# Optimization experiments

Measured on AMD Instinct MI355X. Metric: run time of the kernel, lower is better.

## Reference

```python
import jax, jax.numpy as jnp
import numpy as np

B, N, D_IN, D_OUT, H = 2, 2048, 1024, 1024, 16
HD = D_OUT // H


def setup_inputs() -> dict:
    key = jax.random.key(0)
    ks = jax.random.split(key, 6)
    s_in = 1.0 / np.sqrt(D_IN)
    s_out = 1.0 / np.sqrt(D_OUT)
    return {
        "x": jax.random.normal(ks[0], (B, N, D_IN), dtype=jnp.float32),
        "Wq": jax.random.uniform(ks[1], (D_IN, D_OUT), jnp.float32, -s_in, s_in),
        "Wk": jax.random.uniform(ks[2], (D_IN, D_OUT), jnp.float32, -s_in, s_in),
        "Wv": jax.random.uniform(ks[3], (D_IN, D_OUT), jnp.float32, -s_in, s_in),
        "Wo": jax.random.uniform(ks[4], (D_OUT, D_OUT), jnp.float32, -s_out, s_out),
        "bo": jax.random.uniform(ks[5], (D_OUT,), jnp.float32, -s_out, s_out),
    }


def reference(x, Wq, Wk, Wv, Wo, bo):
    b, n, _ = x.shape
    # project and split heads: [b, n, d_out] -> [b, h, n, hd]
    def heads(w):
        return w.reshape(b, n, H, HD).transpose(0, 2, 1, 3)
    q = heads(x @ Wq)
    k = heads(x @ Wk)
    v = heads(x @ Wv)
    # materialized causal attention (dropout rate 0.0 -> identity)
    scores = jnp.einsum("bhqd,bhkd->bhqk", q, k)
    causal = jnp.tril(jnp.ones((n, n), dtype=bool))  # keep lower triangle
    scores = jnp.where(causal, scores, -jnp.inf)
    attn = jax.nn.softmax(scores / np.sqrt(HD), axis=-1)
    ctx = jnp.einsum("bhqk,bhkd->bhqd", attn, v)
    ctx = ctx.transpose(0, 2, 1, 3).reshape(b, n, D_OUT)
    return ctx @ Wo + bo
```

## Files before the change

kernel.cpp:

```cpp
#include <hip/hip_runtime.h>
#include <math.h>
#include <stdint.h>

#define B_ 2
#define N_ 2048
#define D_ 1024
#define H_ 16
#define HD_ 64
#define M_ (B_ * N_)

typedef __bf16 bf16x8 __attribute__((ext_vector_type(8)));
typedef float f32x4 __attribute__((ext_vector_type(4)));

__device__ __forceinline__ ushort bfbits(float f) {
    __bf16 h = (__bf16)f;
    return __builtin_bit_cast(ushort, h);
}

__device__ __forceinline__ void glds16(const ushort* g, ushort* l) {
    __builtin_amdgcn_global_load_lds(
        (const __attribute__((address_space(1))) uint32_t*)g,
        (__attribute__((address_space(3))) uint32_t*)l, 16, 0, 0);
}

__global__ __launch_bounds__(256) void cvt_x(const float* __restrict__ x,
                                             ushort* __restrict__ xb) {
    int i = blockIdx.x * 256 + threadIdx.x;
    float4 v = ((const float4*)x)[i];
    ushort4 o;
    o.x = bfbits(v.x); o.y = bfbits(v.y); o.z = bfbits(v.z); o.w = bfbits(v.w);
    ((ushort4*)xb)[i] = o;
}

__global__ __launch_bounds__(256) void cvt_w(const float* __restrict__ W0,
                                             const float* __restrict__ W1,
                                             const float* __restrict__ W2,
                                             const float* __restrict__ W3,
                                             ushort* __restrict__ Wt) {
    __shared__ float T[32][33];
    const float* W = (blockIdx.z == 0) ? W0 : (blockIdx.z == 1) ? W1
                   : (blockIdx.z == 2) ? W2 : W3;
    ushort* out = Wt + (size_t)blockIdx.z * D_ * D_;
    const int t = threadIdx.x;
    const int k0 = blockIdx.x * 32, n0 = blockIdx.y * 32;
    {
        int kl = t >> 3, nl = (t & 7) * 4;
        float4 v = *(const float4*)&W[(size_t)(k0 + kl) * D_ + n0 + nl];
        T[kl][nl] = v.x; T[kl][nl + 1] = v.y; T[kl][nl + 2] = v.z; T[kl][nl + 3] = v.w;
    }
    __syncthreads();
    {
        int nl = t >> 3, k4 = (t & 7) * 4;
        ushort4 o;
        o.x = bfbits(T[k4 + 0][nl]); o.y = bfbits(T[k4 + 1][nl]);
        o.z = bfbits(T[k4 + 2][nl]); o.w = bfbits(T[k4 + 3][nl]);
        *(ushort4*)&out[(size_t)(n0 + nl) * D_ + k0 + k4] = o;
    }
}

#define BK 32

__device__ __forceinline__ void gemm_tile(const ushort* __restrict__ A,
                                          const ushort* __restrict__ Bt,
                                          int K, int tileM, int tileN,
                                          ushort* As, ushort* Bs,
                                          f32x4 acc[4][4]) {
    const int t = threadIdx.x;
    const int l = t & 63;
    const int w = __builtin_amdgcn_readfirstlane(t >> 6);
    const int wr = w >> 1, wc = w & 1;
    const int li = l & 15, lg = l >> 4;
    const int lr = l >> 2;
    const int colu = (((l & 3) ^ (lr & 3)) << 3);
    const int swz = (li & 3) << 3;

    for (int k0 = 0; k0 < K; k0 += BK) {
        __syncthreads();
        #pragma unroll
        for (int it = 0; it < 2; ++it) {
            const int c2 = it * 4 + w;
            const int row = c2 * 16 + lr;
            glds16(&A[(size_t)(tileM + row) * K + k0 + colu], &As[c2 * 512]);
            glds16(&Bt[(size_t)(tileN + row) * K + k0 + colu], &Bs[c2 * 512]);
        }
        __syncthreads();
        bf16x8 a[4], b[4];
        #pragma unroll
        for (int m = 0; m < 4; ++m)
            a[m] = *(const bf16x8*)&As[(wr * 64 + m * 16 + li) * 32 + ((lg << 3) ^ swz)];
        #pragma unroll
        for (int n = 0; n < 4; ++n)
            b[n] = *(const bf16x8*)&Bs[(wc * 64 + n * 16 + li) * 32 + ((lg << 3) ^ swz)];
        #pragma unroll
        for (int m = 0; m < 4; ++m)
            #pragma unroll
            for (int n = 0; n < 4; ++n)
                acc[m][n] = __builtin_amdgcn_mfma_f32_16x16x32_bf16(a[m], b[n], acc[m][n], 0, 0, 0);
    }
}

#define QSCALE 0.180336880f

__global__ __launch_bounds__(256) void qkv_gemm(const ushort* __restrict__ xb,
                                                const ushort* __restrict__ Wt,
                                                ushort* __restrict__ q,
                                                ushort* __restrict__ k,
                                                ushort* __restrict__ vt) {
    __shared__ ushort As[128 * 32];
    __shared__ ushort Bs[128 * 32];
    __shared__ ushort Eps[128][130];
    f32x4 acc[4][4];
    #pragma unroll
    for (int m = 0; m < 4; ++m)
        #pragma unroll
        for (int n = 0; n < 4; ++n)
            acc[m][n] = (f32x4){0.f, 0.f, 0.f, 0.f};

    const int tileM = blockIdx.x * 128;
    const int wsel = blockIdx.y >> 3;
    const int tileN = (blockIdx.y & 7) * 128;
    const ushort* Bmat = Wt + (size_t)wsel * D_ * D_;

    gemm_tile(xb, Bmat, D_, tileM, tileN, As, Bs, acc);

    const int t = threadIdx.x;
    const int l = t & 63, w = t >> 6;
    const int wr = w >> 1, wc = w & 1;
    const int li = l & 15, lg = l >> 4;
    const float scale = (wsel == 0) ? QSCALE : 1.0f;

    if (wsel < 2) {
        #pragma unroll
        for (int m = 0; m < 4; ++m)
            #pragma unroll
            for (int n = 0; n < 4; ++n)
                #pragma unroll
                for (int r = 0; r < 4; ++r)
                    Eps[wr * 64 + m * 16 + lg * 4 + r][wc * 64 + n * 16 + li] =
                        bfbits(acc[m][n][r] * scale);
    } else {
        #pragma unroll
        for (int m = 0; m < 4; ++m)
            #pragma unroll
            for (int n = 0; n < 4; ++n)
                #pragma unroll
                for (int r = 0; r < 4; ++r)
                    Eps[wc * 64 + n * 16 + li][wr * 64 + m * 16 + lg * 4 + r] =
                        bfbits(acc[m][n][r]);
    }
    __syncthreads();

    const int rr = t >> 3;
    const int cb = (t & 7) * 16;
    if (wsel < 2) {
        ushort* out = (wsel == 0) ? q : k;
        #pragma unroll
        for (int it = 0; it < 4; ++it) {
            const int row = it * 32 + rr;
            uint4 v0 = *(const uint4*)&Eps[row][cb];
            uint4 v1 = *(const uint4*)&Eps[row][cb + 8];
            size_t base = (size_t)(tileM + row) * D_ + tileN + cb;
            *(uint4*)&out[base] = v0;
            *(uint4*)&out[base + 8] = v1;
        }
    } else {
        const int b = tileM >> 11;
        const int n0 = (tileM & (N_ - 1)) + cb;
        #pragma unroll
        for (int it = 0; it < 4; ++it) {
            const int row = it * 32 + rr;
            const int gcol = tileN + row;
            const int h = gcol >> 6, hd = gcol & 63;
            uint4 v0 = *(const uint4*)&Eps[row][cb];
            uint4 v1 = *(const uint4*)&Eps[row][cb + 8];
            size_t base = ((size_t)(b * H_ + h) * HD_ + hd) * N_ + n0;
            *(uint4*)&vt[base] = v0;
            *(uint4*)&vt[base + 8] = v1;
        }
    }
}

__global__ __launch_bounds__(256) void out_gemm(const ushort* __restrict__ ctx,
                                                const ushort* __restrict__ Wt,
                                                const float* __restrict__ bo,
                                                float* __restrict__ outp) {
    __shared__ ushort As[128 * 32];
    __shared__ ushort Bs[128 * 32];
    __shared__ float Epf[32][132];
    f32x4 acc[4][4];
    #pragma unroll
    for (int m = 0; m < 4; ++m)
        #pragma unroll
        for (int n = 0; n < 4; ++n)
            acc[m][n] = (f32x4){0.f, 0.f, 0.f, 0.f};

    const int tileM = blockIdx.x * 128;
    const int tileN = blockIdx.y * 128;
    const ushort* Bmat = Wt + (size_t)3 * D_ * D_;

    gemm_tile(ctx, Bmat, D_, tileM, tileN, As, Bs, acc);

    const int t = threadIdx.x;
    const int l = t & 63, w = t >> 6;
    const int wr = w >> 1, wc = w & 1;
    const int li = l & 15, lg = l >> 4;
    const int lrow = t & 31;
    const int coff = (t >> 5) * 16;

    float bias[4];
    #pragma unroll
    for (int n = 0; n < 4; ++n) bias[n] = bo[tileN + wc * 64 + n * 16 + li];

    #pragma unroll
    for (int m = 0; m < 4; ++m) {
        __syncthreads();
        #pragma unroll
        for (int n = 0; n < 4; ++n)
            #pragma unroll
            for (int r = 0; r < 4; ++r)
                Epf[wr * 16 + lg * 4 + r][wc * 64 + n * 16 + li] = acc[m][n][r] + bias[n];
        __syncthreads();
        const int grow = tileM + (lrow >> 4) * 64 + m * 16 + (lrow & 15);
        #pragma unroll
        for (int j = 0; j < 4; ++j) {
            float4 vv = *(const float4*)&Epf[lrow][coff + j * 4];
            *(float4*)&outp[(size_t)grow * D_ + tileN + coff + j * 4] = vv;
        }
    }
}

__device__ __forceinline__ void qk_mfma(f32x4 st[4], const ushort* Kb,
                                        const bf16x8 bq[2],
                                        int li, int lg, int rswz) {
    #pragma unroll
    for (int c = 0; c < 4; ++c) {
        st[c] = (f32x4){0.f, 0.f, 0.f, 0.f};
        #pragma unroll
        for (int tk = 0; tk < 2; ++tk) {
            bf16x8 kf = *(const bf16x8*)&Kb[(c * 16 + li) * 64 + (((tk * 4 + lg) ^ rswz) * 8)];
            st[c] = __builtin_amdgcn_mfma_f32_16x16x32_bf16(kf, bq[tk], st[c], 0, 0, 0);
        }
    }
}

__device__ __forceinline__ void softmax_pv(f32x4 st[4], const ushort* Vb,
                                           bool masked, int jkb, int qg,
                                           int li, int lg, int rswz,
                                           ushort* PsW, f32x4& lacc,
                                           f32x4 od[4], bf16x8 ones) {
    if (masked) {
        #pragma unroll
        for (int c = 0; c < 4; ++c)
            #pragma unroll
            for (int r = 0; r < 4; ++r) {
                const int kgl = jkb * 64 + c * 16 + lg * 4 + r;
                if (kgl > qg) st[c][r] = -INFINITY;
            }
    }
    const int sw = li & 7;
    #pragma unroll
    for (int c = 0; c < 4; ++c) {
        float p0 = exp2f(st[c][0]);
        float p1 = exp2f(st[c][1]);
        float p2 = exp2f(st[c][2]);
        float p3 = exp2f(st[c][3]);
        uint32_t w0, w1;
        asm("v_cvt_pk_bf16_f32 %0, %1, %2" : "=v"(w0) : "v"(p0), "v"(p1));
        asm("v_cvt_pk_bf16_f32 %0, %1, %2" : "=v"(w1) : "v"(p2), "v"(p3));
        uint2 pk; pk.x = w0; pk.y = w1;
        *(uint2*)&PsW[li * 64 + (((c * 2 + (lg >> 1)) ^ sw) << 3) + ((lg & 1) << 2)] = pk;
    }
    #pragma unroll
    for (int tj = 0; tj < 2; ++tj) {
        bf16x8 pa = *(const bf16x8*)&PsW[li * 64 + (((tj * 4 + lg) ^ sw) << 3)];
        lacc = __builtin_amdgcn_mfma_f32_16x16x32_bf16(pa, ones, lacc, 0, 0, 0);
        #pragma unroll
        for (int db = 0; db < 4; ++db) {
            bf16x8 bv = *(const bf16x8*)&Vb[(db * 16 + li) * 64 + (((tj * 4 + lg) ^ rswz) * 8)];
            od[db] = __builtin_amdgcn_mfma_f32_16x16x32_bf16(pa, bv, od[db], 0, 0, 0);
        }
    }
}

__global__ __launch_bounds__(256, 4) void attn_fwd(const ushort* __restrict__ q,
                                                   const ushort* __restrict__ k,
                                                   const ushort* __restrict__ vt,
                                                   ushort* __restrict__ ctx) {
    __shared__ ushort Ks[2][4096];
    __shared__ ushort Vs[2][4096];
    __shared__ ushort Ps[4][1024];

    const int t = threadIdx.x;
    const int l = t & 63;
    const int w = __builtin_amdgcn_readfirstlane(t >> 6);
    const int li = l & 15, lg = l >> 4;
    const int f = blockIdx.x;
    const int bh = ((f & 7) << 2) | ((f >> 3) & 3);
    const int qt = 31 - (f >> 5);
    const int b = bh >> 4, h = bh & 15;

    const ushort* Qg = q + ((size_t)b * N_) * D_ + h * 64;
    const ushort* Kg = k + ((size_t)b * N_) * D_ + h * 64;
    const ushort* Vg = vt + (size_t)bh * HD_ * N_;
    ushort* PsW = &Ps[w][0];

    const int r8 = l >> 3;
    const int soff = ((l & 7) ^ r8) * 8;
    const int rswz = li & 7;

    const int qb64 = qt * 64 + w * 16;
    const int qg = qb64 + li;

    bf16x8 bq[2];
    #pragma unroll
    for (int tk = 0; tk < 2; ++tk)
        bq[tk] = *(const bf16x8*)&Qg[(size_t)qg * D_ + tk * 32 + lg * 8];

    bf16x8 ones;
    #pragma unroll
    for (int i = 0; i < 8; ++i) ones[i] = (__bf16)1.0f;

    f32x4 od[4];
    #pragma unroll
    for (int db = 0; db < 4; ++db) od[db] = (f32x4){0.f, 0.f, 0.f, 0.f};
    f32x4 lacc = (f32x4){0.f, 0.f, 0.f, 0.f};

    #pragma unroll
    for (int i = 0; i < 2; ++i) {
        const int seg = w + i * 4;
        const int row = seg * 8 + r8;
        glds16(&Kg[(size_t)row * D_ + soff], &Ks[0][seg * 512]);
        glds16(&Vg[(size_t)row * N_ + soff], &Vs[0][seg * 512]);
    }
    __syncthreads();

    int cur = 0;
    for (int kb = 0; kb < qt; ++kb) {
        #pragma unroll
        for (int i = 0; i < 2; ++i) {
            const int seg = w + i * 4;
            const int row = seg * 8 + r8;
            glds16(&Kg[(size_t)((kb + 1) * 64 + row) * D_ + soff], &Ks[cur ^ 1][seg * 512]);
            glds16(&Vg[(size_t)row * N_ + (kb + 1) * 64 + soff], &Vs[cur ^ 1][seg * 512]);
        }
        f32x4 st[4];
        qk_mfma(st, Ks[cur], bq, li, lg, rswz);
        softmax_pv(st, Vs[cur], false, kb, qg, li, lg, rswz, PsW, lacc, od, ones);
        __syncthreads();
        cur ^= 1;
    }
    {
        f32x4 st[4];
        qk_mfma(st, Ks[cur], bq, li, lg, rswz);
        softmax_pv(st, Vs[cur], true, qt, qg, li, lg, rswz, PsW, lacc, od, ones);
    }

    #pragma unroll
    for (int r = 0; r < 4; ++r) {
        const float inv = 1.f / lacc[r];
        const int grow = qb64 + lg * 4 + r;
        #pragma unroll
        for (int db = 0; db < 4; ++db)
            ctx[((size_t)(b * N_ + grow)) * D_ + h * 64 + db * 16 + li] = bfbits(od[db][r] * inv);
    }
}

extern "C" void kernel_launch(void* const* d_in, const int* in_sizes, int n_in,
                              void* d_out, int out_size, void* d_ws, size_t ws_size,
                              hipStream_t stream) {
    (void)in_sizes; (void)n_in; (void)out_size; (void)ws_size;
    const float* x  = (const float*)d_in[0];
    const float* Wq = (const float*)d_in[1];
    const float* Wk = (const float*)d_in[2];
    const float* Wv = (const float*)d_in[3];
    const float* Wo = (const float*)d_in[4];
    const float* bo = (const float*)d_in[5];
    float* outp = (float*)d_out;

    ushort* xb  = (ushort*)d_ws;
    ushort* Wt  = xb + (size_t)M_ * D_;
    ushort* qb  = Wt + (size_t)4 * D_ * D_;
    ushort* kb  = qb + (size_t)M_ * D_;
    ushort* vtb = kb + (size_t)M_ * D_;
    ushort* ctx = vtb + (size_t)M_ * D_;

    cvt_x<<<dim3((M_ * D_ / 4) / 256), 256, 0, stream>>>(x, xb);
    cvt_w<<<dim3(32, 32, 4), 256, 0, stream>>>(Wq, Wk, Wv, Wo, Wt);
    qkv_gemm<<<dim3(32, 24), 256, 0, stream>>>(xb, Wt, qb, kb, vtb);
    attn_fwd<<<dim3(1024), 256, 0, stream>>>(qb, kb, vtb, ctx);
    out_gemm<<<dim3(32, 8), 256, 0, stream>>>(ctx, Wt, bo, outp);
}
```

Baseline: 111.8 us.

## Rewrite attention with 32x32 MFMA, 128-row query tiles and register P exchange

The attention kernel moves from 16x16x32 to 32x32x16 MFMA and gives each block 128 query rows (interleaved across waves) instead of 64, halving the grid. The probability tile now goes from the S accumulator to the PV operand through permlane32_swap instead of a per-wave LDS round trip, and the row sum comes from scalar adds instead of an MFMA against a ones vector. Query tiles are reordered so long and short causal tiles are paired for load balance. In exchange it uses more registers (launch bounds drop to 2 blocks per CU), and the two diagonal K blocks take extra masking work.

```diff
diff --git a/kernel.cpp b/kernel.cpp
--- a/kernel.cpp
+++ b/kernel.cpp
@@ -11,6 +11,9 @@
 
 typedef __bf16 bf16x8 __attribute__((ext_vector_type(8)));
 typedef float f32x4 __attribute__((ext_vector_type(4)));
+typedef float f32x16 __attribute__((ext_vector_type(16)));
+typedef unsigned int u32x2 __attribute__((ext_vector_type(2)));
+typedef unsigned int u32x4 __attribute__((ext_vector_type(4)));
 
 __device__ __forceinline__ ushort bfbits(float f) {
     __bf16 h = (__bf16)f;
@@ -229,101 +232,45 @@
     }
 }
 
-__device__ __forceinline__ void qk_mfma(f32x4 st[4], const ushort* Kb,
-                                        const bf16x8 bq[2],
-                                        int li, int lg, int rswz) {
-    #pragma unroll
-    for (int c = 0; c < 4; ++c) {
-        st[c] = (f32x4){0.f, 0.f, 0.f, 0.f};
-        #pragma unroll
-        for (int tk = 0; tk < 2; ++tk) {
-            bf16x8 kf = *(const bf16x8*)&Kb[(c * 16 + li) * 64 + (((tk * 4 + lg) ^ rswz) * 8)];
-            st[c] = __builtin_amdgcn_mfma_f32_16x16x32_bf16(kf, bq[tk], st[c], 0, 0, 0);
-        }
-    }
-}
-
-__device__ __forceinline__ void softmax_pv(f32x4 st[4], const ushort* Vb,
-                                           bool masked, int jkb, int qg,
-                                           int li, int lg, int rswz,
-                                           ushort* PsW, f32x4& lacc,
-                                           f32x4 od[4], bf16x8 ones) {
-    if (masked) {
-        #pragma unroll
-        for (int c = 0; c < 4; ++c)
-            #pragma unroll
-            for (int r = 0; r < 4; ++r) {
-                const int kgl = jkb * 64 + c * 16 + lg * 4 + r;
-                if (kgl > qg) st[c][r] = -INFINITY;
-            }
-    }
-    const int sw = li & 7;
-    #pragma unroll
-    for (int c = 0; c < 4; ++c) {
-        float p0 = exp2f(st[c][0]);
-        float p1 = exp2f(st[c][1]);
-        float p2 = exp2f(st[c][2]);
-        float p3 = exp2f(st[c][3]);
-        uint32_t w0, w1;
-        asm("v_cvt_pk_bf16_f32 %0, %1, %2" : "=v"(w0) : "v"(p0), "v"(p1));
-        asm("v_cvt_pk_bf16_f32 %0, %1, %2" : "=v"(w1) : "v"(p2), "v"(p3));
-        uint2 pk; pk.x = w0; pk.y = w1;
-        *(uint2*)&PsW[li * 64 + (((c * 2 + (lg >> 1)) ^ sw) << 3) + ((lg & 1) << 2)] = pk;
-    }
-    #pragma unroll
-    for (int tj = 0; tj < 2; ++tj) {
-        bf16x8 pa = *(const bf16x8*)&PsW[li * 64 + (((tj * 4 + lg) ^ sw) << 3)];
-        lacc = __builtin_amdgcn_mfma_f32_16x16x32_bf16(pa, ones, lacc, 0, 0, 0);
-        #pragma unroll
-        for (int db = 0; db < 4; ++db) {
-            bf16x8 bv = *(const bf16x8*)&Vb[(db * 16 + li) * 64 + (((tj * 4 + lg) ^ rswz) * 8)];
-            od[db] = __builtin_amdgcn_mfma_f32_16x16x32_bf16(pa, bv, od[db], 0, 0, 0);
-        }
-    }
-}
-
-__global__ __launch_bounds__(256, 4) void attn_fwd(const ushort* __restrict__ q,
+__global__ __launch_bounds__(256, 2) void attn_fwd(const ushort* __restrict__ q,
                                                    const ushort* __restrict__ k,
                                                    const ushort* __restrict__ vt,
                                                    ushort* __restrict__ ctx) {
     __shared__ ushort Ks[2][4096];
     __shared__ ushort Vs[2][4096];
-    __shared__ ushort Ps[4][1024];
 
     const int t = threadIdx.x;
     const int l = t & 63;
     const int w = __builtin_amdgcn_readfirstlane(t >> 6);
-    const int li = l & 15, lg = l >> 4;
+    const int l31 = l & 31;
+    const int hi = l >> 5;
     const int f = blockIdx.x;
     const int bh = ((f & 7) << 2) | ((f >> 3) & 3);
-    const int qt = 31 - (f >> 5);
+    const int kq = f >> 5;
+    const int qt = (kq < 8) ? (15 - kq) : (kq - 8);
     const int b = bh >> 4, h = bh & 15;
 
     const ushort* Qg = q + ((size_t)b * N_) * D_ + h * 64;
     const ushort* Kg = k + ((size_t)b * N_) * D_ + h * 64;
     const ushort* Vg = vt + (size_t)bh * HD_ * N_;
-    ushort* PsW = &Ps[w][0];
 
     const int r8 = l >> 3;
     const int soff = ((l & 7) ^ r8) * 8;
-    const int rswz = li & 7;
-
-    const int qb64 = qt * 64 + w * 16;
-    const int qg = qb64 + li;
-
-    bf16x8 bq[2];
-    #pragma unroll
-    for (int tk = 0; tk < 2; ++tk)
-        bq[tk] = *(const bf16x8*)&Qg[(size_t)qg * D_ + tk * 32 + lg * 8];
-
-    bf16x8 ones;
-    #pragma unroll
-    for (int i = 0; i < 8; ++i) ones[i] = (__bf16)1.0f;
-
-    f32x4 od[4];
-    #pragma unroll
-    for (int db = 0; db < 4; ++db) od[db] = (f32x4){0.f, 0.f, 0.f, 0.f};
-    f32x4 lacc = (f32x4){0.f, 0.f, 0.f, 0.f};
+    const int rsw = l & 7;
+
+    const int qg = qt * 128 + 4 * l31 + w;
+
+    bf16x8 bq[4];
+    #pragma unroll
+    for (int tk = 0; tk < 4; ++tk)
+        bq[tk] = *(const bf16x8*)&Qg[(size_t)qg * D_ + tk * 16 + hi * 8];
+
+    f32x16 od[2];
+    od[0] = (f32x16){};
+    od[1] = (f32x16){};
+    float ls = 0.f;
+
+    const int nkb = 2 * qt + 2;
 
     #pragma unroll
     for (int i = 0; i < 2; ++i) {
@@ -335,34 +282,87 @@
     __syncthreads();
 
     int cur = 0;
-    for (int kb = 0; kb < qt; ++kb) {
-        #pragma unroll
-        for (int i = 0; i < 2; ++i) {
-            const int seg = w + i * 4;
-            const int row = seg * 8 + r8;
-            glds16(&Kg[(size_t)((kb + 1) * 64 + row) * D_ + soff], &Ks[cur ^ 1][seg * 512]);
-            glds16(&Vg[(size_t)row * N_ + (kb + 1) * 64 + soff], &Vs[cur ^ 1][seg * 512]);
-        }
-        f32x4 st[4];
-        qk_mfma(st, Ks[cur], bq, li, lg, rswz);
-        softmax_pv(st, Vs[cur], false, kb, qg, li, lg, rswz, PsW, lacc, od, ones);
+    for (int kb = 0; kb < nkb; ++kb) {
+        if (kb + 1 < nkb) {
+            #pragma unroll
+            for (int i = 0; i < 2; ++i) {
+                const int seg = w + i * 4;
+                const int row = seg * 8 + r8;
+                glds16(&Kg[(size_t)((kb + 1) * 64 + row) * D_ + soff], &Ks[cur ^ 1][seg * 512]);
+                glds16(&Vg[(size_t)row * N_ + (kb + 1) * 64 + soff], &Vs[cur ^ 1][seg * 512]);
+            }
+        }
+
+        f32x16 st[2];
+        #pragma unroll
+        for (int j0 = 0; j0 < 2; ++j0) {
+            st[j0] = (f32x16){};
+            #pragma unroll
+            for (int tk = 0; tk < 4; ++tk) {
+                bf16x8 kf = *(const bf16x8*)&Ks[cur][(j0 * 32 + l31) * 64 +
+                                                     (((tk * 2 + hi) ^ rsw) * 8)];
+                st[j0] = __builtin_amdgcn_mfma_f32_32x32x16_bf16(kf, bq[tk], st[j0], 0, 0, 0);
+            }
+        }
+
+        if (kb >= nkb - 2) {
+            #pragma unroll
+            for (int j0 = 0; j0 < 2; ++j0)
+                #pragma unroll
+                for (int r = 0; r < 16; ++r) {
+                    const int key = kb * 64 + j0 * 32 + (r & 3) + 8 * (r >> 2) + 4 * hi;
+                    if (key > qg) st[j0][r] = -INFINITY;
+                }
+        }
+
+        #pragma unroll
+        for (int j0 = 0; j0 < 2; ++j0) {
+            uint32_t pkx[8];
+            #pragma unroll
+            for (int g = 0; g < 4; ++g) {
+                float p0 = exp2f(st[j0][4 * g + 0]);
+                float p1 = exp2f(st[j0][4 * g + 1]);
+                float p2 = exp2f(st[j0][4 * g + 2]);
+                float p3 = exp2f(st[j0][4 * g + 3]);
+                ls += (p0 + p1) + (p2 + p3);
+                asm("v_cvt_pk_bf16_f32 %0, %1, %2" : "=v"(pkx[2 * g]) : "v"(p0), "v"(p1));
+                asm("v_cvt_pk_bf16_f32 %0, %1, %2" : "=v"(pkx[2 * g + 1]) : "v"(p2), "v"(p3));
+            }
+            #pragma unroll
+            for (int par = 0; par < 2; ++par) {
+                u32x2 s0 = __builtin_amdgcn_permlane32_swap(pkx[4 * par + 0], pkx[4 * par + 2], false, false);
+                u32x2 s1 = __builtin_amdgcn_permlane32_swap(pkx[4 * par + 1], pkx[4 * par + 3], false, false);
+                u32x4 fr;
+                fr.x = s0[0]; fr.y = s1[0]; fr.z = s0[1]; fr.w = s1[1];
+                bf16x8 pb = __builtin_bit_cast(bf16x8, fr);
+                const int kslot = 2 * j0 + par;
+                #pragma unroll
+                for (int hd0 = 0; hd0 < 2; ++hd0) {
+                    bf16x8 vf = *(const bf16x8*)&Vs[cur][(hd0 * 32 + l31) * 64 +
+                                                         (((kslot * 2 + hi) ^ rsw) * 8)];
+                    od[hd0] = __builtin_amdgcn_mfma_f32_32x32x16_bf16(vf, pb, od[hd0], 0, 0, 0);
+                }
+            }
+        }
+
         __syncthreads();
         cur ^= 1;
     }
-    {
-        f32x4 st[4];
-        qk_mfma(st, Ks[cur], bq, li, lg, rswz);
-        softmax_pv(st, Vs[cur], true, qt, qg, li, lg, rswz, PsW, lacc, od, ones);
-    }
-
-    #pragma unroll
-    for (int r = 0; r < 4; ++r) {
-        const float inv = 1.f / lacc[r];
-        const int grow = qb64 + lg * 4 + r;
-        #pragma unroll
-        for (int db = 0; db < 4; ++db)
-            ctx[((size_t)(b * N_ + grow)) * D_ + h * 64 + db * 16 + li] = bfbits(od[db][r] * inv);
-    }
+
+    const float lq = ls + __shfl_xor(ls, 32);
+    const float inv = 1.f / lq;
+    ushort* crow = ctx + ((size_t)(b * N_ + qg)) * D_ + h * 64;
+    #pragma unroll
+    for (int hd0 = 0; hd0 < 2; ++hd0)
+        #pragma unroll
+        for (int g = 0; g < 4; ++g) {
+            ushort4 o;
+            o.x = bfbits(od[hd0][4 * g + 0] * inv);
+            o.y = bfbits(od[hd0][4 * g + 1] * inv);
+            o.z = bfbits(od[hd0][4 * g + 2] * inv);
+            o.w = bfbits(od[hd0][4 * g + 3] * inv);
+            *(ushort4*)&crow[hd0 * 32 + 8 * g + 4 * hi] = o;
+        }
 }
 
 extern "C" void kernel_launch(void* const* d_in, const int* in_sizes, int n_in,
@@ -387,6 +387,6 @@
     cvt_x<<<dim3((M_ * D_ / 4) / 256), 256, 0, stream>>>(x, xb);
     cvt_w<<<dim3(32, 32, 4), 256, 0, stream>>>(Wq, Wk, Wv, Wo, Wt);
     qkv_gemm<<<dim3(32, 24), 256, 0, stream>>>(xb, Wt, qb, kb, vtb);
-    attn_fwd<<<dim3(1024), 256, 0, stream>>>(qb, kb, vtb, ctx);
+    attn_fwd<<<dim3(512), 256, 0, stream>>>(qb, kb, vtb, ctx);
     out_gemm<<<dim3(32, 8), 256, 0, stream>>>(ctx, Wt, bo, outp);
 }
```

After: 118.2 us. 1.06x slower.
